# Performance work log

Hardware: AMD Instinct MI355X
Metric: run time of the kernel (lower is better)

The kernel has to match this reference:

```python
import jax, jax.numpy as jnp
import numpy as np

# Model/config dims
N_NODE = 500000   # num_node (item vocab)
D      = 100      # opt.hiddenSize
B      = 512      # batch
S      = 50       # session seq len
NS     = 12       # opt.n_sample neighbors per node
HOP    = 1        # opt.n_iter
STEP   = 1        # opt.step (star-graph propagation steps)
LAST   = 3        # opt.last_len
NADJ   = 12       # adjacent items per last item
SCALE  = 1.0 / np.sqrt(D)


def setup_inputs() -> dict:
    key = jax.random.key(0)
    ks = jax.random.split(key, 16)
    stdv = 1.0 / np.sqrt(D)
    u = lambda k, sh: jax.random.uniform(k, sh, jnp.float32, -stdv, stdv)
    return {
        # forward args
        "inputs":     jax.random.randint(ks[0], (B, S), 0, N_NODE),
        "adj":        jax.random.uniform(ks[1], (B, S, S), jnp.float32),
        "item":       jax.random.randint(ks[2], (B, S), 0, N_NODE),
        "last_items": jax.random.randint(ks[3], (B, LAST), 0, N_NODE),
        "adj_items":  jax.random.randint(ks[4], (B, LAST * NADJ), 0, N_NODE),
        # learned params / buffers
        "embedding": u(ks[5], (N_NODE, D)),
        "s":         u(ks[6], (2, 1)),
        "W_star_a":  u(ks[7], (D, D)),
        "W_star_q":  u(ks[8], (D, D)),
        "W_star_k":  u(ks[9], (D, D)),
        "W_g":       u(ks[10], (2 * D, D)),
        "W_l":       u(ks[11], (D, D)),
        "adj_all":   jax.random.randint(ks[12], (N_NODE, NS), 0, N_NODE),
        "num_w":     jax.random.uniform(ks[13], (N_NODE, NS), jnp.float32),
    }


def _l2norm(x):
    # F.normalize(p=2, dim=-1)
    return x / jnp.maximum(jnp.linalg.norm(x, axis=-1, keepdims=True), 1e-12)


def reference(inputs, adj, item, last_items, adj_items,
              embedding, s, W_star_a, W_star_q, W_star_k, W_g, W_l,
              adj_all, num_w):
    # ----- embedding lookup + padding mask -----
    h = embedding[inputs]                                  # [B,S,D]
    mask = (inputs != 0).astype(h.dtype)                   # [B,S]

    # ----- StarAggregator (local branch): star node + gated propagation -----
    denom = jnp.maximum(mask.sum(-1, keepdims=True), 1.0)
    star = (h * mask[..., None]).sum(1) / denom            # [B,D] masked mean
    hl = h
    for _ in range(STEP):
        h_n = jnp.einsum('bst,btd->bsd', adj, hl @ W_star_a)          # neighbor agg
        gate = jax.nn.sigmoid(
            jnp.einsum('bsd,bd->bs', hl @ W_star_q, star @ W_star_k) * SCALE)
        hl = (1.0 - gate)[..., None] * h_n + gate[..., None] * star[:, None, :]
        beta = jnp.einsum('bsd,bd->bs', hl, star) * SCALE
        beta = jax.nn.softmax(jnp.where(mask > 0, beta, -1e9), axis=1)
        star = jnp.einsum('bs,bsd->bd', beta, hl)
    h_local = hl                                           # [B,S,D]

    # ----- GlobalAggregator (hop=1 neighbor-sampling branch) -----
    flat = inputs.reshape(-1)
    neigh_idx = adj_all[flat].reshape(B, S, NS)            # gathered neighbor ids
    neigh_w = num_w[flat].reshape(B, S, NS)                # co-occurrence weights
    neigh = embedding[neigh_idx]                           # [B,S,NS,D]
    alpha = jax.nn.softmax(neigh_w, axis=-1)
    agg = jnp.einsum('bsn,bsnd->bsd', alpha, neigh)        # weighted neighbor sum
    h_global = jax.nn.relu(jnp.concatenate([h, agg], -1) @ W_g)  # [B,S,D]

    # ----- normalize + (eval-mode dropout = identity) + learned 2-way combine -----
    h_local = _l2norm(h_local)
    h_global = _l2norm(h_global)
    output = jnp.einsum('bsdk,ko->bsdo',
                        jnp.stack([h_local, h_global], axis=-1), s)[..., 0]  # [B,S,D]

    # ----- LastAggregator (last-items attention branch) -----
    item_h = embedding[last_items]                         # [B,L,D]
    adj_h = embedding[adj_items].reshape(B, LAST, -1, D)   # [B,L,NADJ,D]
    q = item_h @ W_l
    att = jax.nn.softmax(jnp.einsum('bld,blnd->bln', q, adj_h) * SCALE, axis=-1)
    aggl = jnp.einsum('bln,blnd->bld', att, adj_h)
    last_hidden = (item_h + aggl).mean(axis=1)             # [B,D]

    return output, last_hidden
```

## Files before the change

kernel.cpp:

```cpp
#include <hip/hip_runtime.h>

#define B_    512
#define S_    50
#define D_    100
#define NS_   12
#define LAST_ 3
#define NADJ_ 12
#define SCALE_ 0.1f

__global__ __launch_bounds__(256, 3) void fused_all(
    const int* __restrict__ inputs,
    const float* __restrict__ adj,
    const float* __restrict__ emb,
    const int* __restrict__ adj_all,
    const float* __restrict__ num_w,
    const float* __restrict__ sW,
    const float* __restrict__ Wa,
    const float* __restrict__ Wq,
    const float* __restrict__ Wk,
    const float* __restrict__ Wg,
    const int* __restrict__ last_items,
    const int* __restrict__ adj_items,
    const float* __restrict__ Wl,
    float* __restrict__ out)
{
    __shared__ __align__(16) float hL[S_][D_];
    __shared__ __align__(16) float hwa[S_][D_];
    __shared__ __align__(16) float ssq[S_][25];
    __shared__ float star[D_], kb[D_], kq[D_];
    __shared__ float gate[S_], rinv[S_], rinv2[S_];
    __shared__ int   ids[S_];
    __shared__ int   nid[S_ * NS_];
    __shared__ float alf[S_ * NS_];
    __shared__ float denom;

    const int t = threadIdx.x;

    if (blockIdx.x >= B_) {
        const int b = blockIdx.x - B_;
        float* ih  = &hL[0][0];
        float* ah  = &hL[0][0] + 304;
        float* qL  = &hwa[0][0];
        float* att = &ssq[0][0];
        int*   li  = ids;
        int*   ai  = nid;

        if (t < LAST_) li[t] = last_items[b * LAST_ + t];
        if (t < LAST_ * NADJ_) ai[t] = adj_items[b * LAST_ * NADJ_ + t];
        __syncthreads();

        for (int e = t; e < LAST_ * 25; e += 256) {
            int l = e / 25, dq = e - l * 25;
            ((float4*)ih)[e] = ((const float4*)(emb + li[l] * D_))[dq];
        }
        for (int e = t; e < LAST_ * NADJ_ * 25; e += 256) {
            int j = e / 25, dq = e - j * 25;
            ((float4*)ah)[e] = ((const float4*)(emb + ai[j] * D_))[dq];
        }
        __syncthreads();

        for (int e = t; e < LAST_ * D_; e += 256) {
            int l = e / D_, d = e - l * D_;
            float a = 0.f;
            for (int k = 0; k < D_; ++k) a = fmaf(ih[l * D_ + k], Wl[k * D_ + d], a);
            qL[e] = a;
        }
        __syncthreads();

        if (t < LAST_ * NADJ_) {
            int l = t / NADJ_;
            const float* ar = ah + t * D_;
            const float* qr = qL + l * D_;
            float a = 0.f;
            for (int d = 0; d < D_; ++d) a = fmaf(qr[d], ar[d], a);
            att[t] = a * SCALE_;
        }
        __syncthreads();

        if (t < LAST_) {
            float mx = -1e30f;
            for (int n = 0; n < NADJ_; ++n) mx = fmaxf(mx, att[t * NADJ_ + n]);
            float ex[NADJ_]; float sm = 0.f;
            for (int n = 0; n < NADJ_; ++n) { ex[n] = expf(att[t * NADJ_ + n] - mx); sm += ex[n]; }
            float inv = 1.f / sm;
            for (int n = 0; n < NADJ_; ++n) att[t * NADJ_ + n] = ex[n] * inv;
        }
        __syncthreads();

        if (t < D_) {
            float acc = 0.f;
            for (int l = 0; l < LAST_; ++l) {
                float a = ih[l * D_ + t];
                for (int n = 0; n < NADJ_; ++n)
                    a = fmaf(att[l * NADJ_ + n], ah[(l * NADJ_ + n) * D_ + t], a);
                acc += a;
            }
            out[B_ * S_ * D_ + b * D_ + t] = acc * (1.f / 3.f);
        }
        return;
    }

    const int b = blockIdx.x;
    const float s0 = sW[0], s1 = sW[1];

    if (t < S_) ids[t] = inputs[b * S_ + t];
    __syncthreads();

    if (t < 64) {
        unsigned long long m = __ballot(t < S_ && ids[t] != 0);
        if (t == 0) denom = fmaxf((float)__popcll(m), 1.f);
    }
    for (int e = t; e < S_ * 25; e += 256) {
        int s = e / 25, dq = e - s * 25;
        ((float4*)&hL[0][0])[e] = ((const float4*)(emb + ids[s] * D_))[dq];
    }
    for (int e = t; e < S_ * NS_; e += 256) {
        int r = e / NS_, n = e - r * NS_;
        nid[e] = adj_all[ids[r] * NS_ + n];
        alf[e] = num_w[ids[r] * NS_ + n];
    }
    __syncthreads();

    if (t < D_) {
        float a = 0.f;
        for (int s = 0; s < S_; ++s) a += (ids[s] != 0) ? hL[s][t] : 0.f;
        star[t] = a / denom;
    } else if (t >= 128 && t < 128 + S_) {
        int r = t - 128;
        float mx = -1e30f;
#pragma unroll
        for (int n = 0; n < NS_; ++n) mx = fmaxf(mx, alf[r * NS_ + n]);
        float ex[NS_]; float sm = 0.f;
#pragma unroll
        for (int n = 0; n < NS_; ++n) { ex[n] = expf(alf[r * NS_ + n] - mx); sm += ex[n]; }
        float inv = 1.f / sm;
#pragma unroll
        for (int n = 0; n < NS_; ++n) alf[r * NS_ + n] = ex[n] * inv;
    }
    __syncthreads();

    if (t < D_) {
        float a = 0.f;
        for (int k = 0; k < D_; ++k) a = fmaf(star[k], Wk[k * D_ + t], a);
        kb[t] = a;
    }
    __syncthreads();

    if (t < D_) {
        float a = 0.f;
        const float4* wr = (const float4*)(Wq + t * D_);
#pragma unroll 5
        for (int j = 0; j < 25; ++j) {
            float4 u = wr[j]; int k = j * 4;
            a = fmaf(u.x, kb[k + 0], a); a = fmaf(u.y, kb[k + 1], a);
            a = fmaf(u.z, kb[k + 2], a); a = fmaf(u.w, kb[k + 3], a);
        }
        kq[t] = a;
    }
    __syncthreads();

    if (t < S_) {
        float a = 0.f;
        const float4* hr = (const float4*)&hL[t][0];
#pragma unroll 5
        for (int j = 0; j < 25; ++j) {
            float4 u = hr[j]; int k = j * 4;
            a = fmaf(u.x, kq[k + 0], a); a = fmaf(u.y, kq[k + 1], a);
            a = fmaf(u.z, kq[k + 2], a); a = fmaf(u.w, kq[k + 3], a);
        }
        gate[t] = 1.f / (1.f + expf(-a * SCALE_));
    }

    const bool act = (t < 250);
    int sg = 0, dg = 0, sb = 0, d4 = 0;
    if (act) { sg = t / 25; dg = t - sg * 25; sb = sg * 5; d4 = dg * 4; }

    if (act) {
        float acc[5][4] = {};
        const float4* WaQ = (const float4*)Wa;
        for (int k = 0; k < D_; k += 4) {
            float4 w0 = WaQ[(k + 0) * 25 + dg];
            float4 w1 = WaQ[(k + 1) * 25 + dg];
            float4 w2 = WaQ[(k + 2) * 25 + dg];
            float4 w3 = WaQ[(k + 3) * 25 + dg];
#pragma unroll
            for (int i = 0; i < 5; ++i) {
                float4 x = *(const float4*)&hL[sb + i][k];
                acc[i][0] = fmaf(x.x,w0.x, fmaf(x.y,w1.x, fmaf(x.z,w2.x, fmaf(x.w,w3.x, acc[i][0]))));
                acc[i][1] = fmaf(x.x,w0.y, fmaf(x.y,w1.y, fmaf(x.z,w2.y, fmaf(x.w,w3.y, acc[i][1]))));
                acc[i][2] = fmaf(x.x,w0.z, fmaf(x.y,w1.z, fmaf(x.z,w2.z, fmaf(x.w,w3.z, acc[i][2]))));
                acc[i][3] = fmaf(x.x,w0.w, fmaf(x.y,w1.w, fmaf(x.z,w2.w, fmaf(x.w,w3.w, acc[i][3]))));
            }
        }
#pragma unroll
        for (int i = 0; i < 5; ++i) {
            float4 v; v.x = acc[i][0]; v.y = acc[i][1]; v.z = acc[i][2]; v.w = acc[i][3];
            *(float4*)&hwa[sb + i][d4] = v;
        }
    }
    __syncthreads();

    float hl[5][4] = {};
    if (act) {
        const float* adjp = adj + b * S_ * S_;
        for (int k = 0; k < S_; k += 2) {
            float4 w0 = *(const float4*)&hwa[k][d4];
            float4 w1 = *(const float4*)&hwa[k + 1][d4];
#pragma unroll
            for (int i = 0; i < 5; ++i) {
                float2 a2 = *(const float2*)(adjp + (sb + i) * S_ + k);
                hl[i][0] = fmaf(a2.x, w0.x, fmaf(a2.y, w1.x, hl[i][0]));
                hl[i][1] = fmaf(a2.x, w0.y, fmaf(a2.y, w1.y, hl[i][1]));
                hl[i][2] = fmaf(a2.x, w0.z, fmaf(a2.y, w1.z, hl[i][2]));
                hl[i][3] = fmaf(a2.x, w0.w, fmaf(a2.y, w1.w, hl[i][3]));
            }
        }
#pragma unroll
        for (int i = 0; i < 5; ++i) {
            float g = gate[sb + i];
#pragma unroll
            for (int j = 0; j < 4; ++j)
                hl[i][j] = (1.f - g) * hl[i][j] + g * star[d4 + j];
            ssq[sb + i][dg] = hl[i][0]*hl[i][0] + hl[i][1]*hl[i][1]
                            + hl[i][2]*hl[i][2] + hl[i][3]*hl[i][3];
        }
    }
    __syncthreads();

    if (t < S_) {
        float ss = 0.f;
#pragma unroll
        for (int j = 0; j < 25; ++j) ss += ssq[t][j];
        rinv[t] = s0 / fmaxf(sqrtf(ss), 1e-12f);
    }
    __syncthreads();

    if (act) {
#pragma unroll
        for (int i = 0; i < 5; ++i) {
            float f = rinv[sb + i];
#pragma unroll
            for (int j = 0; j < 4; ++j) hl[i][j] *= f;
        }
#pragma unroll
        for (int i = 0; i < 5; ++i) {
            int row = sb + i;
            float a0 = 0.f, a1 = 0.f, a2 = 0.f, a3 = 0.f;
#pragma unroll
            for (int n = 0; n < NS_; ++n) {
                float4 u = ((const float4*)(emb + nid[row * NS_ + n] * D_))[dg];
                float al = alf[row * NS_ + n];
                a0 = fmaf(al, u.x, a0); a1 = fmaf(al, u.y, a1);
                a2 = fmaf(al, u.z, a2); a3 = fmaf(al, u.w, a3);
            }
            float4 v; v.x = a0; v.y = a1; v.z = a2; v.w = a3;
            *(float4*)&hwa[row][d4] = v;
        }
    }
    __syncthreads();

    float o[5][4] = {};
    if (act) {
        const float4* WgQ = (const float4*)Wg;
        for (int k = 0; k < D_; k += 4) {
            float4 w0 = WgQ[(k + 0) * 25 + dg];
            float4 w1 = WgQ[(k + 1) * 25 + dg];
            float4 w2 = WgQ[(k + 2) * 25 + dg];
            float4 w3 = WgQ[(k + 3) * 25 + dg];
#pragma unroll
            for (int i = 0; i < 5; ++i) {
                float4 x = *(const float4*)&hL[sb + i][k];
                o[i][0] = fmaf(x.x,w0.x, fmaf(x.y,w1.x, fmaf(x.z,w2.x, fmaf(x.w,w3.x, o[i][0]))));
                o[i][1] = fmaf(x.x,w0.y, fmaf(x.y,w1.y, fmaf(x.z,w2.y, fmaf(x.w,w3.y, o[i][1]))));
                o[i][2] = fmaf(x.x,w0.z, fmaf(x.y,w1.z, fmaf(x.z,w2.z, fmaf(x.w,w3.z, o[i][2]))));
                o[i][3] = fmaf(x.x,w0.w, fmaf(x.y,w1.w, fmaf(x.z,w2.w, fmaf(x.w,w3.w, o[i][3]))));
            }
        }
        for (int k = 0; k < D_; k += 4) {
            float4 w0 = WgQ[(D_ + k + 0) * 25 + dg];
            float4 w1 = WgQ[(D_ + k + 1) * 25 + dg];
            float4 w2 = WgQ[(D_ + k + 2) * 25 + dg];
            float4 w3 = WgQ[(D_ + k + 3) * 25 + dg];
#pragma unroll
            for (int i = 0; i < 5; ++i) {
                float4 x = *(const float4*)&hwa[sb + i][k];
                o[i][0] = fmaf(x.x,w0.x, fmaf(x.y,w1.x, fmaf(x.z,w2.x, fmaf(x.w,w3.x, o[i][0]))));
                o[i][1] = fmaf(x.x,w0.y, fmaf(x.y,w1.y, fmaf(x.z,w2.y, fmaf(x.w,w3.y, o[i][1]))));
                o[i][2] = fmaf(x.x,w0.z, fmaf(x.y,w1.z, fmaf(x.z,w2.z, fmaf(x.w,w3.z, o[i][2]))));
                o[i][3] = fmaf(x.x,w0.w, fmaf(x.y,w1.w, fmaf(x.z,w2.w, fmaf(x.w,w3.w, o[i][3]))));
            }
        }
#pragma unroll
        for (int i = 0; i < 5; ++i) {
#pragma unroll
            for (int j = 0; j < 4; ++j) o[i][j] = fmaxf(o[i][j], 0.f);
            ssq[sb + i][dg] = o[i][0]*o[i][0] + o[i][1]*o[i][1]
                            + o[i][2]*o[i][2] + o[i][3]*o[i][3];
        }
    }
    __syncthreads();

    if (t < S_) {
        float ss = 0.f;
#pragma unroll
        for (int j = 0; j < 25; ++j) ss += ssq[t][j];
        rinv2[t] = s1 / fmaxf(sqrtf(ss), 1e-12f);
    }
    __syncthreads();

    if (act) {
#pragma unroll
        for (int i = 0; i < 5; ++i) {
            float f = rinv2[sb + i];
            int row = b * S_ + sb + i;
            float4 ov;
            ov.x = hl[i][0] + o[i][0] * f;
            ov.y = hl[i][1] + o[i][1] * f;
            ov.z = hl[i][2] + o[i][2] * f;
            ov.w = hl[i][3] + o[i][3] * f;
            ((float4*)(out + row * D_))[dg] = ov;
        }
    }
}

extern "C" void kernel_launch(void* const* d_in, const int* in_sizes, int n_in,
                              void* d_out, int out_size, void* d_ws, size_t ws_size,
                              hipStream_t stream) {
    (void)in_sizes; (void)n_in; (void)out_size; (void)d_ws; (void)ws_size;
    const int* inputs     = (const int*)d_in[0];
    const float* adj      = (const float*)d_in[1];
    const int* last_items = (const int*)d_in[3];
    const int* adj_items  = (const int*)d_in[4];
    const float* emb      = (const float*)d_in[5];
    const float* sW       = (const float*)d_in[6];
    const float* Wa       = (const float*)d_in[7];
    const float* Wq       = (const float*)d_in[8];
    const float* Wk       = (const float*)d_in[9];
    const float* Wg       = (const float*)d_in[10];
    const float* Wl       = (const float*)d_in[11];
    const int* adj_all    = (const int*)d_in[12];
    const float* num_w    = (const float*)d_in[13];

    float* out = (float*)d_out;

    fused_all<<<2 * B_, 256, 0, stream>>>(inputs, adj, emb, adj_all, num_w,
                                          sW, Wa, Wq, Wk, Wg,
                                          last_items, adj_items, Wl, out);
}
```

Baseline: 360.8 us.

## Stage adj in shared fp16, prefetch weights, merge syncs, use fast exp

The kernel now copies each batch's adj matrix into shared memory as half precision (sharing storage with the ssq buffer through a union) instead of reading it from global memory inside the propagation loop. The Wa and Wg GEMM loops are software-pipelined, loading the next weight rows while the current ones are used, and the first Wa loads are hoisted to before the embedding gather. The local-branch norm reduction is moved after the neighbor gather so one barrier pair is dropped, and expf is replaced with __expf. Converting adj to fp16 and using the fast exp both reduce precision, and the extra live registers may lower occupancy.

```diff
diff --git a/kernel.cpp b/kernel.cpp
--- a/kernel.cpp
+++ b/kernel.cpp
@@ -1,4 +1,5 @@
 #include <hip/hip_runtime.h>
+#include <hip/hip_fp16.h>
 
 #define B_    512
 #define S_    50
@@ -7,6 +8,16 @@
 #define LAST_ 3
 #define NADJ_ 12
 #define SCALE_ 0.1f
+
+#define GEMM_STEP(ACC, BUF, K, W0, W1, W2, W3)                                      \
+    _Pragma("unroll")                                                                \
+    for (int i = 0; i < 5; ++i) {                                                    \
+        float4 x = *(const float4*)&BUF[sb + i][K];                                  \
+        ACC[i][0] = fmaf(x.x,W0.x, fmaf(x.y,W1.x, fmaf(x.z,W2.x, fmaf(x.w,W3.x, ACC[i][0])))); \
+        ACC[i][1] = fmaf(x.x,W0.y, fmaf(x.y,W1.y, fmaf(x.z,W2.y, fmaf(x.w,W3.y, ACC[i][1])))); \
+        ACC[i][2] = fmaf(x.x,W0.z, fmaf(x.y,W1.z, fmaf(x.z,W2.z, fmaf(x.w,W3.z, ACC[i][2])))); \
+        ACC[i][3] = fmaf(x.x,W0.w, fmaf(x.y,W1.w, fmaf(x.z,W2.w, fmaf(x.w,W3.w, ACC[i][3])))); \
+    }
 
 __global__ __launch_bounds__(256, 3) void fused_all(
     const int* __restrict__ inputs,
@@ -26,7 +37,10 @@
 {
     __shared__ __align__(16) float hL[S_][D_];
     __shared__ __align__(16) float hwa[S_][D_];
-    __shared__ __align__(16) float ssq[S_][25];
+    __shared__ __align__(16) union UAS {
+        __half adjH[S_][S_];
+        float  ssq[S_][25];
+    } u;
     __shared__ float star[D_], kb[D_], kq[D_];
     __shared__ float gate[S_], rinv[S_], rinv2[S_];
     __shared__ int   ids[S_];
@@ -41,7 +55,7 @@
         float* ih  = &hL[0][0];
         float* ah  = &hL[0][0] + 304;
         float* qL  = &hwa[0][0];
-        float* att = &ssq[0][0];
+        float* att = &u.ssq[0][0];
         int*   li  = ids;
         int*   ai  = nid;
 
@@ -81,7 +95,7 @@
             float mx = -1e30f;
             for (int n = 0; n < NADJ_; ++n) mx = fmaxf(mx, att[t * NADJ_ + n]);
             float ex[NADJ_]; float sm = 0.f;
-            for (int n = 0; n < NADJ_; ++n) { ex[n] = expf(att[t * NADJ_ + n] - mx); sm += ex[n]; }
+            for (int n = 0; n < NADJ_; ++n) { ex[n] = __expf(att[t * NADJ_ + n] - mx); sm += ex[n]; }
             float inv = 1.f / sm;
             for (int n = 0; n < NADJ_; ++n) att[t * NADJ_ + n] = ex[n] * inv;
         }
@@ -103,6 +117,17 @@
     const int b = blockIdx.x;
     const float s0 = sW[0], s1 = sW[1];
 
+    const bool act = (t < 250);
+    int sg = 0, dg = 0, sb = 0, d4 = 0;
+    if (act) { sg = t / 25; dg = t - sg * 25; sb = sg * 5; d4 = dg * 4; }
+
+    const float4* WaQ = (const float4*)Wa;
+    float4 wa0, wa1, wa2, wa3;
+    if (act) {
+        wa0 = WaQ[0 * 25 + dg]; wa1 = WaQ[1 * 25 + dg];
+        wa2 = WaQ[2 * 25 + dg]; wa3 = WaQ[3 * 25 + dg];
+    }
+
     if (t < S_) ids[t] = inputs[b * S_ + t];
     __syncthreads();
 
@@ -113,6 +138,15 @@
     for (int e = t; e < S_ * 25; e += 256) {
         int s = e / 25, dq = e - s * 25;
         ((float4*)&hL[0][0])[e] = ((const float4*)(emb + ids[s] * D_))[dq];
+    }
+    {
+        __half2* dst = (__half2*)&u.adjH[0][0];
+        const float4* src = (const float4*)(adj + b * S_ * S_);
+        for (int e = t; e < S_ * S_ / 4; e += 256) {
+            float4 v = src[e];
+            dst[2 * e]     = __floats2half2_rn(v.x, v.y);
+            dst[2 * e + 1] = __floats2half2_rn(v.z, v.w);
+        }
     }
     for (int e = t; e < S_ * NS_; e += 256) {
         int r = e / NS_, n = e - r * NS_;
@@ -132,7 +166,7 @@
         for (int n = 0; n < NS_; ++n) mx = fmaxf(mx, alf[r * NS_ + n]);
         float ex[NS_]; float sm = 0.f;
 #pragma unroll
-        for (int n = 0; n < NS_; ++n) { ex[n] = expf(alf[r * NS_ + n] - mx); sm += ex[n]; }
+        for (int n = 0; n < NS_; ++n) { ex[n] = __expf(alf[r * NS_ + n] - mx); sm += ex[n]; }
         float inv = 1.f / sm;
 #pragma unroll
         for (int n = 0; n < NS_; ++n) alf[r * NS_ + n] = ex[n] * inv;
@@ -151,9 +185,9 @@
         const float4* wr = (const float4*)(Wq + t * D_);
 #pragma unroll 5
         for (int j = 0; j < 25; ++j) {
-            float4 u = wr[j]; int k = j * 4;
-            a = fmaf(u.x, kb[k + 0], a); a = fmaf(u.y, kb[k + 1], a);
-            a = fmaf(u.z, kb[k + 2], a); a = fmaf(u.w, kb[k + 3], a);
+            float4 uq = wr[j]; int k = j * 4;
+            a = fmaf(uq.x, kb[k + 0], a); a = fmaf(uq.y, kb[k + 1], a);
+            a = fmaf(uq.z, kb[k + 2], a); a = fmaf(uq.w, kb[k + 3], a);
         }
         kq[t] = a;
     }
@@ -164,34 +198,22 @@
         const float4* hr = (const float4*)&hL[t][0];
 #pragma unroll 5
         for (int j = 0; j < 25; ++j) {
-            float4 u = hr[j]; int k = j * 4;
-            a = fmaf(u.x, kq[k + 0], a); a = fmaf(u.y, kq[k + 1], a);
-            a = fmaf(u.z, kq[k + 2], a); a = fmaf(u.w, kq[k + 3], a);
-        }
-        gate[t] = 1.f / (1.f + expf(-a * SCALE_));
-    }
-
-    const bool act = (t < 250);
-    int sg = 0, dg = 0, sb = 0, d4 = 0;
-    if (act) { sg = t / 25; dg = t - sg * 25; sb = sg * 5; d4 = dg * 4; }
+            float4 uq = hr[j]; int k = j * 4;
+            a = fmaf(uq.x, kq[k + 0], a); a = fmaf(uq.y, kq[k + 1], a);
+            a = fmaf(uq.z, kq[k + 2], a); a = fmaf(uq.w, kq[k + 3], a);
+        }
+        gate[t] = 1.f / (1.f + __expf(-a * SCALE_));
+    }
 
     if (act) {
         float acc[5][4] = {};
-        const float4* WaQ = (const float4*)Wa;
-        for (int k = 0; k < D_; k += 4) {
-            float4 w0 = WaQ[(k + 0) * 25 + dg];
-            float4 w1 = WaQ[(k + 1) * 25 + dg];
-            float4 w2 = WaQ[(k + 2) * 25 + dg];
-            float4 w3 = WaQ[(k + 3) * 25 + dg];
-#pragma unroll
-            for (int i = 0; i < 5; ++i) {
-                float4 x = *(const float4*)&hL[sb + i][k];
-                acc[i][0] = fmaf(x.x,w0.x, fmaf(x.y,w1.x, fmaf(x.z,w2.x, fmaf(x.w,w3.x, acc[i][0]))));
-                acc[i][1] = fmaf(x.x,w0.y, fmaf(x.y,w1.y, fmaf(x.z,w2.y, fmaf(x.w,w3.y, acc[i][1]))));
-                acc[i][2] = fmaf(x.x,w0.z, fmaf(x.y,w1.z, fmaf(x.z,w2.z, fmaf(x.w,w3.z, acc[i][2]))));
-                acc[i][3] = fmaf(x.x,w0.w, fmaf(x.y,w1.w, fmaf(x.z,w2.w, fmaf(x.w,w3.w, acc[i][3]))));
-            }
-        }
+        for (int k = 0; k < 96; k += 4) {
+            float4 n0 = WaQ[(k + 4) * 25 + dg], n1 = WaQ[(k + 5) * 25 + dg],
+                   n2 = WaQ[(k + 6) * 25 + dg], n3 = WaQ[(k + 7) * 25 + dg];
+            GEMM_STEP(acc, hL, k, wa0, wa1, wa2, wa3)
+            wa0 = n0; wa1 = n1; wa2 = n2; wa3 = n3;
+        }
+        GEMM_STEP(acc, hL, 96, wa0, wa1, wa2, wa3)
 #pragma unroll
         for (int i = 0; i < 5; ++i) {
             float4 v; v.x = acc[i][0]; v.y = acc[i][1]; v.z = acc[i][2]; v.w = acc[i][3];
@@ -202,13 +224,12 @@
 
     float hl[5][4] = {};
     if (act) {
-        const float* adjp = adj + b * S_ * S_;
         for (int k = 0; k < S_; k += 2) {
             float4 w0 = *(const float4*)&hwa[k][d4];
             float4 w1 = *(const float4*)&hwa[k + 1][d4];
 #pragma unroll
             for (int i = 0; i < 5; ++i) {
-                float2 a2 = *(const float2*)(adjp + (sb + i) * S_ + k);
+                float2 a2 = __half22float2(*(const __half2*)&u.adjH[sb + i][k]);
                 hl[i][0] = fmaf(a2.x, w0.x, fmaf(a2.y, w1.x, hl[i][0]));
                 hl[i][1] = fmaf(a2.x, w0.y, fmaf(a2.y, w1.y, hl[i][1]));
                 hl[i][2] = fmaf(a2.x, w0.z, fmaf(a2.y, w1.z, hl[i][2]));
@@ -221,37 +242,29 @@
 #pragma unroll
             for (int j = 0; j < 4; ++j)
                 hl[i][j] = (1.f - g) * hl[i][j] + g * star[d4 + j];
-            ssq[sb + i][dg] = hl[i][0]*hl[i][0] + hl[i][1]*hl[i][1]
-                            + hl[i][2]*hl[i][2] + hl[i][3]*hl[i][3];
-        }
-    }
-    __syncthreads();
-
-    if (t < S_) {
-        float ss = 0.f;
-#pragma unroll
-        for (int j = 0; j < 25; ++j) ss += ssq[t][j];
-        rinv[t] = s0 / fmaxf(sqrtf(ss), 1e-12f);
-    }
-    __syncthreads();
-
-    if (act) {
-#pragma unroll
-        for (int i = 0; i < 5; ++i) {
-            float f = rinv[sb + i];
-#pragma unroll
-            for (int j = 0; j < 4; ++j) hl[i][j] *= f;
-        }
+        }
+    }
+    __syncthreads();
+
+    const float4* WgQ = (const float4*)Wg;
+    float4 wg0, wg1, wg2, wg3;
+    if (act) {
+        wg0 = WgQ[0 * 25 + dg]; wg1 = WgQ[1 * 25 + dg];
+        wg2 = WgQ[2 * 25 + dg]; wg3 = WgQ[3 * 25 + dg];
+#pragma unroll
+        for (int i = 0; i < 5; ++i)
+            u.ssq[sb + i][dg] = hl[i][0]*hl[i][0] + hl[i][1]*hl[i][1]
+                              + hl[i][2]*hl[i][2] + hl[i][3]*hl[i][3];
 #pragma unroll
         for (int i = 0; i < 5; ++i) {
             int row = sb + i;
             float a0 = 0.f, a1 = 0.f, a2 = 0.f, a3 = 0.f;
 #pragma unroll
             for (int n = 0; n < NS_; ++n) {
-                float4 u = ((const float4*)(emb + nid[row * NS_ + n] * D_))[dg];
+                float4 uq = ((const float4*)(emb + nid[row * NS_ + n] * D_))[dg];
                 float al = alf[row * NS_ + n];
-                a0 = fmaf(al, u.x, a0); a1 = fmaf(al, u.y, a1);
-                a2 = fmaf(al, u.z, a2); a3 = fmaf(al, u.w, a3);
+                a0 = fmaf(al, uq.x, a0); a1 = fmaf(al, uq.y, a1);
+                a2 = fmaf(al, uq.z, a2); a3 = fmaf(al, uq.w, a3);
             }
             float4 v; v.x = a0; v.y = a1; v.z = a2; v.w = a3;
             *(float4*)&hwa[row][d4] = v;
@@ -259,51 +272,55 @@
     }
     __syncthreads();
 
-    float o[5][4] = {};
-    if (act) {
-        const float4* WgQ = (const float4*)Wg;
-        for (int k = 0; k < D_; k += 4) {
-            float4 w0 = WgQ[(k + 0) * 25 + dg];
-            float4 w1 = WgQ[(k + 1) * 25 + dg];
-            float4 w2 = WgQ[(k + 2) * 25 + dg];
-            float4 w3 = WgQ[(k + 3) * 25 + dg];
-#pragma unroll
-            for (int i = 0; i < 5; ++i) {
-                float4 x = *(const float4*)&hL[sb + i][k];
-                o[i][0] = fmaf(x.x,w0.x, fmaf(x.y,w1.x, fmaf(x.z,w2.x, fmaf(x.w,w3.x, o[i][0]))));
-                o[i][1] = fmaf(x.x,w0.y, fmaf(x.y,w1.y, fmaf(x.z,w2.y, fmaf(x.w,w3.y, o[i][1]))));
-                o[i][2] = fmaf(x.x,w0.z, fmaf(x.y,w1.z, fmaf(x.z,w2.z, fmaf(x.w,w3.z, o[i][2]))));
-                o[i][3] = fmaf(x.x,w0.w, fmaf(x.y,w1.w, fmaf(x.z,w2.w, fmaf(x.w,w3.w, o[i][3]))));
-            }
-        }
-        for (int k = 0; k < D_; k += 4) {
-            float4 w0 = WgQ[(D_ + k + 0) * 25 + dg];
-            float4 w1 = WgQ[(D_ + k + 1) * 25 + dg];
-            float4 w2 = WgQ[(D_ + k + 2) * 25 + dg];
-            float4 w3 = WgQ[(D_ + k + 3) * 25 + dg];
-#pragma unroll
-            for (int i = 0; i < 5; ++i) {
-                float4 x = *(const float4*)&hwa[sb + i][k];
-                o[i][0] = fmaf(x.x,w0.x, fmaf(x.y,w1.x, fmaf(x.z,w2.x, fmaf(x.w,w3.x, o[i][0]))));
-                o[i][1] = fmaf(x.x,w0.y, fmaf(x.y,w1.y, fmaf(x.z,w2.y, fmaf(x.w,w3.y, o[i][1]))));
-                o[i][2] = fmaf(x.x,w0.z, fmaf(x.y,w1.z, fmaf(x.z,w2.z, fmaf(x.w,w3.z, o[i][2]))));
-                o[i][3] = fmaf(x.x,w0.w, fmaf(x.y,w1.w, fmaf(x.z,w2.w, fmaf(x.w,w3.w, o[i][3]))));
-            }
-        }
-#pragma unroll
-        for (int i = 0; i < 5; ++i) {
-#pragma unroll
-            for (int j = 0; j < 4; ++j) o[i][j] = fmaxf(o[i][j], 0.f);
-            ssq[sb + i][dg] = o[i][0]*o[i][0] + o[i][1]*o[i][1]
-                            + o[i][2]*o[i][2] + o[i][3]*o[i][3];
-        }
-    }
-    __syncthreads();
-
     if (t < S_) {
         float ss = 0.f;
 #pragma unroll
-        for (int j = 0; j < 25; ++j) ss += ssq[t][j];
+        for (int j = 0; j < 25; ++j) ss += u.ssq[t][j];
+        rinv[t] = s0 / fmaxf(sqrtf(ss), 1e-12f);
+    }
+    __syncthreads();
+
+    float o[5][4] = {};
+    if (act) {
+#pragma unroll
+        for (int i = 0; i < 5; ++i) {
+            float f = rinv[sb + i];
+#pragma unroll
+            for (int j = 0; j < 4; ++j) hl[i][j] *= f;
+        }
+        for (int k = 0; k < 96; k += 4) {
+            float4 n0 = WgQ[(k + 4) * 25 + dg], n1 = WgQ[(k + 5) * 25 + dg],
+                   n2 = WgQ[(k + 6) * 25 + dg], n3 = WgQ[(k + 7) * 25 + dg];
+            GEMM_STEP(o, hL, k, wg0, wg1, wg2, wg3)
+            wg0 = n0; wg1 = n1; wg2 = n2; wg3 = n3;
+        }
+        {
+            float4 n0 = WgQ[100 * 25 + dg], n1 = WgQ[101 * 25 + dg],
+                   n2 = WgQ[102 * 25 + dg], n3 = WgQ[103 * 25 + dg];
+            GEMM_STEP(o, hL, 96, wg0, wg1, wg2, wg3)
+            wg0 = n0; wg1 = n1; wg2 = n2; wg3 = n3;
+        }
+        for (int k = 0; k < 96; k += 4) {
+            float4 n0 = WgQ[(100 + k + 4) * 25 + dg], n1 = WgQ[(100 + k + 5) * 25 + dg],
+                   n2 = WgQ[(100 + k + 6) * 25 + dg], n3 = WgQ[(100 + k + 7) * 25 + dg];
+            GEMM_STEP(o, hwa, k, wg0, wg1, wg2, wg3)
+            wg0 = n0; wg1 = n1; wg2 = n2; wg3 = n3;
+        }
+        GEMM_STEP(o, hwa, 96, wg0, wg1, wg2, wg3)
+#pragma unroll
+        for (int i = 0; i < 5; ++i) {
+#pragma unroll
+            for (int j = 0; j < 4; ++j) o[i][j] = fmaxf(o[i][j], 0.f);
+            u.ssq[sb + i][dg] = o[i][0]*o[i][0] + o[i][1]*o[i][1]
+                              + o[i][2]*o[i][2] + o[i][3]*o[i][3];
+        }
+    }
+    __syncthreads();
+
+    if (t < S_) {
+        float ss = 0.f;
+#pragma unroll
+        for (int j = 0; j < 25; ++j) ss += u.ssq[t][j];
         rinv2[t] = s1 / fmaxf(sqrtf(ss), 1e-12f);
     }
     __syncthreads();
```

After: 353.4 us. 2.1% less time.
